# Kernel tuning notes

Hardware: AMD Instinct MI355X
Metric: run time of the kernel (lower is better)

The kernel has to match this reference:

```python
import jax, jax.numpy as jnp
import numpy as np

H, W = 32, 32
S = H * W            # 1024 tokens
B = 16
C = 256              # in_channels == out_channels
HEAD_DIM = 32
N_HEADS = C // HEAD_DIM      # 8
DIM = N_HEADS * HEAD_DIM     # 256
SCALE = DIM ** (-0.5)        # NOTE: full dim, as in the source


def _relative_position_index(h, w):
    # Faithful port of get_relative_position_index (numpy, static)
    coords = np.stack(np.meshgrid(np.arange(h), np.arange(w), indexing='ij'))  # [2,h,w]
    coords_flat = coords.reshape(2, -1)                                        # [2,S]
    rel = coords_flat[:, :, None] - coords_flat[:, None, :]                    # [2,S,S]
    rel = rel.transpose(1, 2, 0).copy()                                        # [S,S,2]
    rel[:, :, 0] += h - 1
    rel[:, :, 1] += w - 1
    rel[:, :, 0] *= 2 * w - 1
    return rel.sum(-1).reshape(-1).astype(np.int32)                            # [S*S]


def setup_inputs() -> dict:
    key = jax.random.key(0)
    ks = jax.random.split(key, 6)
    x = jax.random.normal(ks[0], (B, S, C), dtype=jnp.float32)
    w_qkv = jax.random.normal(ks[1], (3 * DIM, C), dtype=jnp.float32) * 0.02
    b_qkv = jnp.zeros((3 * DIM,), dtype=jnp.float32)
    w_merge = jax.random.normal(ks[2], (C, DIM), dtype=jnp.float32) * 0.02
    b_merge = jnp.zeros((C,), dtype=jnp.float32)
    rel_table = jax.random.normal(ks[3], ((2 * H - 1) * (2 * W - 1), N_HEADS), dtype=jnp.float32) * 0.02
    rel_index = jnp.asarray(_relative_position_index(H, W))  # [S*S] int32
    return {"x": x, "w_qkv": w_qkv, "b_qkv": b_qkv,
            "w_merge": w_merge, "b_merge": b_merge,
            "rel_table": rel_table, "rel_index": rel_index}


def reference(x, w_qkv, b_qkv, w_merge, b_merge, rel_table, rel_index):
    b = x.shape[0]
    qkv = x @ w_qkv.T + b_qkv                       # [B,S,3*DIM]
    q, k, v = jnp.split(qkv, 3, axis=-1)
    def heads(t):
        return t.reshape(b, S, N_HEADS, HEAD_DIM).transpose(0, 2, 1, 3)  # [B,H,S,D]
    q, k, v = heads(q), heads(k), heads(v)
    score = jnp.einsum('bhqd,bhkd->bhqk', q, k) * SCALE   # [B,H,S,S]
    # Faithful to source: torch.gather with index [S*S,1] reads column 0 only
    pos_bias = rel_table[rel_index, 0].reshape(1, 1, S, S)
    attn = jax.nn.softmax(score + pos_bias, axis=-1)
    out = jnp.einsum('bhqk,bhkd->bqhd', attn, v).reshape(b, S, DIM)
    return out @ w_merge.T + b_merge                # [B,S,C]
```

## Files before the change

### kernel.cpp

```cpp
#include <hip/hip_runtime.h>


typedef __attribute__((ext_vector_type(8))) short bf16x8;
typedef __attribute__((ext_vector_type(4))) float f32x4;

#define INV_LN2 1.44269504088896340736f

__device__ __forceinline__ unsigned short f2bf(float f) {
  union { float f; unsigned u; } v; v.f = f;
  unsigned r = v.u + 0x7fffu + ((v.u >> 16) & 1u);
  return (unsigned short)(r >> 16);
}
__device__ __forceinline__ float bf2f(unsigned short h) {
  union { unsigned u; float f; } v; v.u = ((unsigned)h) << 16;
  return v.f;
}

__global__ __launch_bounds__(256) void prep_kernel(
    const float* __restrict__ x, const float* __restrict__ wq,
    const float* __restrict__ wm, const float* __restrict__ tab,
    const int* __restrict__ idx,
    unsigned short* __restrict__ xb, unsigned short* __restrict__ wqb,
    unsigned short* __restrict__ wmb, unsigned short* __restrict__ biasb) {
  const long NX = 1048576, NW1 = 49152, NW2 = 16384, NB = 262144;
  long u = (long)blockIdx.x * 256 + threadIdx.x;
  if (u < NX) {
    float4 v = ((const float4*)x)[u];
    ushort4 o; o.x = f2bf(v.x); o.y = f2bf(v.y); o.z = f2bf(v.z); o.w = f2bf(v.w);
    ((ushort4*)xb)[u] = o;
  } else if (u < NX + NW1) {
    long t = u - NX;
    float4 v = ((const float4*)wq)[t];
    ushort4 o; o.x = f2bf(v.x); o.y = f2bf(v.y); o.z = f2bf(v.z); o.w = f2bf(v.w);
    ((ushort4*)wqb)[t] = o;
  } else if (u < NX + NW1 + NW2) {
    long t = u - NX - NW1;
    float4 v = ((const float4*)wm)[t];
    ushort4 o; o.x = f2bf(v.x); o.y = f2bf(v.y); o.z = f2bf(v.z); o.w = f2bf(v.w);
    ((ushort4*)wmb)[t] = o;
  } else if (u < NX + NW1 + NW2 + NB) {
    long t = (u - NX - NW1 - NW2) * 4;
    int4 iv = ((const int4*)idx)[(u - NX - NW1 - NW2)];
    ushort4 o;
    o.x = f2bf(tab[(long)iv.x * 8] * INV_LN2);
    o.y = f2bf(tab[(long)iv.y * 8] * INV_LN2);
    o.z = f2bf(tab[(long)iv.z * 8] * INV_LN2);
    o.w = f2bf(tab[(long)iv.w * 8] * INV_LN2);
    ((ushort4*)biasb)[t / 4] = o;
  }
}

template <int MODE>
__global__ __launch_bounds__(256) void gemm_k(
    const unsigned short* __restrict__ A, const unsigned short* __restrict__ Bw,
    const float* __restrict__ bias,
    unsigned short* __restrict__ q_ws, unsigned short* __restrict__ k_ws,
    unsigned short* __restrict__ v_ws, float* __restrict__ out) {
  __shared__ unsigned short As[128 * 32];
  __shared__ unsigned short Bs[128 * 32];
  const int tid = threadIdx.x;
  const int lane = tid & 63, wid = tid >> 6;
  const int wm = wid >> 1, wn = wid & 1;
  const int li = lane & 15, g = lane >> 4;
  const int m0 = blockIdx.y * 128;
  const int n0 = blockIdx.x * 128;
  f32x4 acc[4][4] = {};
  const int srow = tid >> 2, sg = tid & 3;
  const unsigned short* Ag = A + (long)(m0 + srow) * 256 + sg * 8;
  const unsigned short* Bg = Bw + (long)(n0 + srow) * 256 + sg * 8;

  for (int kt = 0; kt < 8; ++kt) {
    const int k0 = kt * 32;
    bf16x8 a0 = *(const bf16x8*)(Ag + k0);
    bf16x8 a1 = *(const bf16x8*)(Ag + 64 * 256 + k0);
    bf16x8 b0 = *(const bf16x8*)(Bg + k0);
    bf16x8 b1 = *(const bf16x8*)(Bg + 64 * 256 + k0);
    __syncthreads();
    ((bf16x8*)As)[tid] = a0;
    ((bf16x8*)As)[256 + tid] = a1;
    ((bf16x8*)Bs)[tid] = b0;
    ((bf16x8*)Bs)[256 + tid] = b1;
    __syncthreads();
    bf16x8 af[4], bfr[4];
#pragma unroll
    for (int mi = 0; mi < 4; mi++)
      af[mi] = *(const bf16x8*)(As + (wm * 64 + mi * 16 + li) * 32 + g * 8);
#pragma unroll
    for (int ni = 0; ni < 4; ni++)
      bfr[ni] = *(const bf16x8*)(Bs + (wn * 64 + ni * 16 + li) * 32 + g * 8);
#pragma unroll
    for (int mi = 0; mi < 4; mi++)
#pragma unroll
      for (int ni = 0; ni < 4; ni++)
        acc[mi][ni] = __builtin_amdgcn_mfma_f32_16x16x32_bf16(af[mi], bfr[ni], acc[mi][ni], 0, 0, 0);
  }

  if (MODE == 0) {
    const int sec = n0 >> 8;
    unsigned short* dst = (sec == 0) ? q_ws : ((sec == 1) ? k_ws : v_ws);
#pragma unroll
    for (int mi = 0; mi < 4; mi++)
#pragma unroll
      for (int ni = 0; ni < 4; ni++)
#pragma unroll
        for (int i = 0; i < 4; i++) {
          int m = m0 + wm * 64 + mi * 16 + g * 4 + i;
          int n = n0 + wn * 64 + ni * 16 + li;
          float val = acc[mi][ni][i] + bias[n];
          if (sec == 0) val *= 0.0625f;
          int h = (n >> 5) & 7, d = n & 31;
          int b = m >> 10, s = m & 1023;
          dst[((long)(b * 8 + h) * 1024 + s) * 32 + d] = f2bf(val);
        }
  } else {
#pragma unroll
    for (int mi = 0; mi < 4; mi++)
#pragma unroll
      for (int ni = 0; ni < 4; ni++)
#pragma unroll
        for (int i = 0; i < 4; i++) {
          int m = m0 + wm * 64 + mi * 16 + g * 4 + i;
          int n = n0 + wn * 64 + ni * 16 + li;
          out[(long)m * 256 + n] = acc[mi][ni][i] + bias[n];
        }
  }
}

__global__ __launch_bounds__(256) void attn_kernel(
    const unsigned short* __restrict__ q_ws, const unsigned short* __restrict__ k_ws,
    const unsigned short* __restrict__ v_ws, const unsigned short* __restrict__ biasb,
    unsigned short* __restrict__ attno) {
  __shared__ unsigned short Ks[64 * 32];
  __shared__ unsigned short Vt[32 * 64];
  __shared__ unsigned short Ps[4][16 * 72];
  const int tid = threadIdx.x;
  const int lane = tid & 63, wid = tid >> 6;
  const int li = lane & 15, g = lane >> 4;
  const int bh = blockIdx.y;
  const int q0 = blockIdx.x * 64 + wid * 16;
  const unsigned short* qb = q_ws + (long)bh * 1024 * 32;
  const unsigned short* kb = k_ws + (long)bh * 1024 * 32;
  const unsigned short* vb = v_ws + (long)bh * 1024 * 32;

  bf16x8 qf = *(const bf16x8*)(qb + (q0 + li) * 32 + g * 8);

  f32x4 o0 = {}, o1 = {};
  float lsum[4] = {0.f, 0.f, 0.f, 0.f};
  const int vtok = tid >> 2, vd0 = (tid & 3) * 8;
  const int vswz = (tid & 3) << 4;

  for (int kv0 = 0; kv0 < 1024; kv0 += 64) {
    bf16x8 kv8 = *(const bf16x8*)(kb + (kv0 + (tid >> 2)) * 32 + (tid & 3) * 8);
    bf16x8 vv8 = *(const bf16x8*)(vb + (kv0 + vtok) * 32 + vd0);
    __syncthreads();
    ((bf16x8*)Ks)[tid] = kv8;
#pragma unroll
    for (int j = 0; j < 8; j++) {
      int byteoff = (vd0 + j) * 128 + ((vtok * 2) ^ vswz);
      *(unsigned short*)((char*)Vt + byteoff) = (unsigned short)(unsigned)(unsigned short)vv8[j];
    }
    __syncthreads();

    f32x4 sc[4];
#pragma unroll
    for (int c = 0; c < 4; c++) {
      bf16x8 kf = *(const bf16x8*)(Ks + (c * 16 + li) * 32 + g * 8);
      f32x4 z = {};
      sc[c] = __builtin_amdgcn_mfma_f32_16x16x32_bf16(qf, kf, z, 0, 0, 0);
    }

#pragma unroll
    for (int c = 0; c < 4; c++)
#pragma unroll
      for (int i = 0; i < 4; i++) {
        int qrow = g * 4 + i;
        float bl2 = bf2f(biasb[(long)(q0 + qrow) * 1024 + kv0 + c * 16 + li]);
        float p = exp2f(fmaf(sc[c][i], INV_LN2, bl2));
        lsum[i] += p;
        Ps[wid][qrow * 72 + c * 16 + li] = f2bf(p);
      }

#pragma unroll
    for (int c2 = 0; c2 < 2; c2++) {
      bf16x8 pa = *(const bf16x8*)(&Ps[wid][li * 72 + c2 * 32 + g * 8]);
#pragma unroll
      for (int dblk = 0; dblk < 2; dblk++) {
        int d = li + dblk * 16;
        int byteoff = d * 128 + ((c2 * 64 + g * 16) ^ (((d >> 3) & 3) << 4));
        bf16x8 vf = *(const bf16x8*)((char*)Vt + byteoff);
        if (dblk == 0)
          o0 = __builtin_amdgcn_mfma_f32_16x16x32_bf16(pa, vf, o0, 0, 0, 0);
        else
          o1 = __builtin_amdgcn_mfma_f32_16x16x32_bf16(pa, vf, o1, 0, 0, 0);
      }
    }
  }

#pragma unroll
  for (int i = 0; i < 4; i++) {
    float v = lsum[i];
    v += __shfl_xor(v, 1, 64);
    v += __shfl_xor(v, 2, 64);
    v += __shfl_xor(v, 4, 64);
    v += __shfl_xor(v, 8, 64);
    lsum[i] = v;
  }
  const int b = bh >> 3, h = bh & 7;
#pragma unroll
  for (int i = 0; i < 4; i++) {
    int srow = q0 + g * 4 + i;
    float inv = 1.0f / lsum[i];
    long base = ((long)(b * 1024 + srow)) * 256 + h * 32;
    attno[base + li] = f2bf(o0[i] * inv);
    attno[base + 16 + li] = f2bf(o1[i] * inv);
  }
}

extern "C" void kernel_launch(void* const* d_in, const int* in_sizes, int n_in,
                              void* d_out, int out_size, void* d_ws, size_t ws_size,
                              hipStream_t stream) {
  const float* x      = (const float*)d_in[0];
  const float* wqkv   = (const float*)d_in[1];
  const float* bqkv   = (const float*)d_in[2];
  const float* wmerge = (const float*)d_in[3];
  const float* bmerge = (const float*)d_in[4];
  const float* rtab   = (const float*)d_in[5];
  const int*   ridx   = (const int*)d_in[6];
  float* out = (float*)d_out;

  char* ws = (char*)d_ws;
  unsigned short* xb    = (unsigned short*)(ws);
  unsigned short* wqb   = (unsigned short*)(ws + 8388608);
  unsigned short* wmb   = (unsigned short*)(ws + 8781824);
  unsigned short* biasb = (unsigned short*)(ws + 8912896);
  unsigned short* q_ws  = (unsigned short*)(ws + 11010048);
  unsigned short* k_ws  = (unsigned short*)(ws + 19398656);
  unsigned short* v_ws  = (unsigned short*)(ws + 27787264);
  unsigned short* attno = (unsigned short*)(ws + 36175872);

  prep_kernel<<<5376, 256, 0, stream>>>(x, wqkv, wmerge, rtab, ridx, xb, wqb, wmb, biasb);
  gemm_k<0><<<dim3(6, 128), 256, 0, stream>>>(xb, wqb, bqkv, q_ws, k_ws, v_ws, nullptr);
  attn_kernel<<<dim3(16, 128), 256, 0, stream>>>(q_ws, k_ws, v_ws, biasb, attno);
  gemm_k<1><<<dim3(2, 128), 256, 0, stream>>>(attno, wmb, bmerge, nullptr, nullptr, nullptr, out);
}
```

Baseline: 109.6 us.

## Pre-transpose V, stage bias in LDS, fold softmax sums into MFMA

Adds a separate kernel that writes V transposed into the workspace, so attention loads V tiles with vector reads instead of scattered 16-bit LDS stores. The positional bias is loaded into LDS with coalesced vector loads and fed as the initial MFMA accumulator, and the 1/ln2 factor is folded into the Q scaling so exp2 can be applied directly. Row sums are computed by an extra MFMA against a ones vector, and P is packed with v_cvt_pk_bf16_f32. GEMM and attention LDS tiles are padded to reduce bank conflicts. The cost is one extra kernel launch plus a full pass over V in global memory.

```diff
diff --git a/kernel.cpp b/kernel.cpp
--- a/kernel.cpp
+++ b/kernel.cpp
@@ -39,14 +39,14 @@
     ushort4 o; o.x = f2bf(v.x); o.y = f2bf(v.y); o.z = f2bf(v.z); o.w = f2bf(v.w);
     ((ushort4*)wmb)[t] = o;
   } else if (u < NX + NW1 + NW2 + NB) {
-    long t = (u - NX - NW1 - NW2) * 4;
-    int4 iv = ((const int4*)idx)[(u - NX - NW1 - NW2)];
+    long t = u - NX - NW1 - NW2;
+    int4 iv = ((const int4*)idx)[t];
     ushort4 o;
     o.x = f2bf(tab[(long)iv.x * 8] * INV_LN2);
     o.y = f2bf(tab[(long)iv.y * 8] * INV_LN2);
     o.z = f2bf(tab[(long)iv.z * 8] * INV_LN2);
     o.w = f2bf(tab[(long)iv.w * 8] * INV_LN2);
-    ((ushort4*)biasb)[t / 4] = o;
+    ((ushort4*)biasb)[t] = o;
   }
 }
 
@@ -56,8 +56,8 @@
     const float* __restrict__ bias,
     unsigned short* __restrict__ q_ws, unsigned short* __restrict__ k_ws,
     unsigned short* __restrict__ v_ws, float* __restrict__ out) {
-  __shared__ unsigned short As[128 * 32];
-  __shared__ unsigned short Bs[128 * 32];
+  __shared__ __align__(16) unsigned short As[128 * 40];
+  __shared__ __align__(16) unsigned short Bs[128 * 40];
   const int tid = threadIdx.x;
   const int lane = tid & 63, wid = tid >> 6;
   const int wm = wid >> 1, wn = wid & 1;
@@ -76,18 +76,18 @@
     bf16x8 b0 = *(const bf16x8*)(Bg + k0);
     bf16x8 b1 = *(const bf16x8*)(Bg + 64 * 256 + k0);
     __syncthreads();
-    ((bf16x8*)As)[tid] = a0;
-    ((bf16x8*)As)[256 + tid] = a1;
-    ((bf16x8*)Bs)[tid] = b0;
-    ((bf16x8*)Bs)[256 + tid] = b1;
+    *(bf16x8*)(As + srow * 40 + sg * 8) = a0;
+    *(bf16x8*)(As + (srow + 64) * 40 + sg * 8) = a1;
+    *(bf16x8*)(Bs + srow * 40 + sg * 8) = b0;
+    *(bf16x8*)(Bs + (srow + 64) * 40 + sg * 8) = b1;
     __syncthreads();
     bf16x8 af[4], bfr[4];
 #pragma unroll
     for (int mi = 0; mi < 4; mi++)
-      af[mi] = *(const bf16x8*)(As + (wm * 64 + mi * 16 + li) * 32 + g * 8);
+      af[mi] = *(const bf16x8*)(As + (wm * 64 + mi * 16 + li) * 40 + g * 8);
 #pragma unroll
     for (int ni = 0; ni < 4; ni++)
-      bfr[ni] = *(const bf16x8*)(Bs + (wn * 64 + ni * 16 + li) * 32 + g * 8);
+      bfr[ni] = *(const bf16x8*)(Bs + (wn * 64 + ni * 16 + li) * 40 + g * 8);
 #pragma unroll
     for (int mi = 0; mi < 4; mi++)
 #pragma unroll
@@ -98,6 +98,7 @@
   if (MODE == 0) {
     const int sec = n0 >> 8;
     unsigned short* dst = (sec == 0) ? q_ws : ((sec == 1) ? k_ws : v_ws);
+    const float qscale = 0.0625f * INV_LN2;
 #pragma unroll
     for (int mi = 0; mi < 4; mi++)
 #pragma unroll
@@ -107,7 +108,7 @@
           int m = m0 + wm * 64 + mi * 16 + g * 4 + i;
           int n = n0 + wn * 64 + ni * 16 + li;
           float val = acc[mi][ni][i] + bias[n];
-          if (sec == 0) val *= 0.0625f;
+          if (sec == 0) val *= qscale;
           int h = (n >> 5) & 7, d = n & 31;
           int b = m >> 10, s = m & 1023;
           dst[((long)(b * 8 + h) * 1024 + s) * 32 + d] = f2bf(val);
@@ -126,90 +127,109 @@
   }
 }
 
+__global__ __launch_bounds__(256) void vtrans_kernel(
+    const unsigned short* __restrict__ v, unsigned short* __restrict__ vt) {
+  long u = (long)blockIdx.x * 256 + threadIdx.x;
+  if (u >= 524288) return;
+  int tok_lin = (int)(u >> 2);
+  int dchunk = ((int)u & 3) * 8;
+  int bh = tok_lin >> 10, s = tok_lin & 1023;
+  bf16x8 r = *(const bf16x8*)(v + (long)tok_lin * 32 + dchunk);
+  unsigned short* base = vt + (long)bh * 32768 + s;
+#pragma unroll
+  for (int j = 0; j < 8; j++) base[(long)(dchunk + j) * 1024] = (unsigned short)r[j];
+}
+
 __global__ __launch_bounds__(256) void attn_kernel(
     const unsigned short* __restrict__ q_ws, const unsigned short* __restrict__ k_ws,
-    const unsigned short* __restrict__ v_ws, const unsigned short* __restrict__ biasb,
+    const unsigned short* __restrict__ vt_ws, const unsigned short* __restrict__ biasb,
     unsigned short* __restrict__ attno) {
-  __shared__ unsigned short Ks[64 * 32];
-  __shared__ unsigned short Vt[32 * 64];
-  __shared__ unsigned short Ps[4][16 * 72];
+  __shared__ __align__(16) unsigned short Ks[64 * 40];
+  __shared__ __align__(16) unsigned short Vt[32 * 72];
+  __shared__ __align__(16) unsigned short Bi[64 * 72];
+  __shared__ __align__(16) unsigned short Ps[4][16 * 72];
   const int tid = threadIdx.x;
   const int lane = tid & 63, wid = tid >> 6;
   const int li = lane & 15, g = lane >> 4;
   const int bh = blockIdx.y;
-  const int q0 = blockIdx.x * 64 + wid * 16;
-  const unsigned short* qb = q_ws + (long)bh * 1024 * 32;
-  const unsigned short* kb = k_ws + (long)bh * 1024 * 32;
-  const unsigned short* vb = v_ws + (long)bh * 1024 * 32;
+  const int qblk = blockIdx.x * 64;
+  const int q0 = qblk + wid * 16;
+  const unsigned short* qb = q_ws + (long)bh * 32768;
+  const unsigned short* kb = k_ws + (long)bh * 32768;
+  const unsigned short* vb = vt_ws + (long)bh * 32768;
 
   bf16x8 qf = *(const bf16x8*)(qb + (q0 + li) * 32 + g * 8);
 
-  f32x4 o0 = {}, o1 = {};
-  float lsum[4] = {0.f, 0.f, 0.f, 0.f};
-  const int vtok = tid >> 2, vd0 = (tid & 3) * 8;
-  const int vswz = (tid & 3) << 4;
+  bf16x8 onesf = {};
+  if (li == 0) {
+#pragma unroll
+    for (int j = 0; j < 8; j++) onesf[j] = (short)0x3F80;
+  }
+
+  f32x4 o0 = {}, o1 = {}, o2 = {};
+  const int kt = tid >> 2, kd = (tid & 3) * 8;
+  const int vd = tid >> 3, vs = (tid & 7) * 8;
+  const int bq = tid >> 2, bt = (tid & 3) * 16;
+  unsigned short* Pw = Ps[wid];
 
   for (int kv0 = 0; kv0 < 1024; kv0 += 64) {
-    bf16x8 kv8 = *(const bf16x8*)(kb + (kv0 + (tid >> 2)) * 32 + (tid & 3) * 8);
-    bf16x8 vv8 = *(const bf16x8*)(vb + (kv0 + vtok) * 32 + vd0);
-    __syncthreads();
-    ((bf16x8*)Ks)[tid] = kv8;
-#pragma unroll
-    for (int j = 0; j < 8; j++) {
-      int byteoff = (vd0 + j) * 128 + ((vtok * 2) ^ vswz);
-      *(unsigned short*)((char*)Vt + byteoff) = (unsigned short)(unsigned)(unsigned short)vv8[j];
+    bf16x8 kv8 = *(const bf16x8*)(kb + (kv0 + kt) * 32 + kd);
+    bf16x8 vv8 = *(const bf16x8*)(vb + vd * 1024 + kv0 + vs);
+    bf16x8 bb0 = *(const bf16x8*)(biasb + (long)(qblk + bq) * 1024 + kv0 + bt);
+    bf16x8 bb1 = *(const bf16x8*)(biasb + (long)(qblk + bq) * 1024 + kv0 + bt + 8);
+    __syncthreads();
+    *(bf16x8*)(Ks + kt * 40 + kd) = kv8;
+    *(bf16x8*)(Vt + vd * 72 + vs) = vv8;
+    *(bf16x8*)(Bi + bq * 72 + bt) = bb0;
+    *(bf16x8*)(Bi + bq * 72 + bt + 8) = bb1;
+    __syncthreads();
+
+    f32x4 sc[4];
+#pragma unroll
+    for (int c = 0; c < 4; c++) {
+      const unsigned short* brow = Bi + (wid * 16 + g * 4) * 72 + c * 16 + li;
+      f32x4 ci;
+      ci[0] = bf2f(brow[0]);
+      ci[1] = bf2f(brow[72]);
+      ci[2] = bf2f(brow[144]);
+      ci[3] = bf2f(brow[216]);
+      bf16x8 kf = *(const bf16x8*)(Ks + (c * 16 + li) * 40 + g * 8);
+      sc[c] = __builtin_amdgcn_mfma_f32_16x16x32_bf16(qf, kf, ci, 0, 0, 0);
     }
-    __syncthreads();
-
-    f32x4 sc[4];
+
 #pragma unroll
     for (int c = 0; c < 4; c++) {
-      bf16x8 kf = *(const bf16x8*)(Ks + (c * 16 + li) * 32 + g * 8);
-      f32x4 z = {};
-      sc[c] = __builtin_amdgcn_mfma_f32_16x16x32_bf16(qf, kf, z, 0, 0, 0);
+      float p0 = exp2f(sc[c][0]);
+      float p1 = exp2f(sc[c][1]);
+      float p2 = exp2f(sc[c][2]);
+      float p3 = exp2f(sc[c][3]);
+      unsigned r01, r23;
+      asm("v_cvt_pk_bf16_f32 %0, %1, %2" : "=v"(r01) : "v"(p0), "v"(p1));
+      asm("v_cvt_pk_bf16_f32 %0, %1, %2" : "=v"(r23) : "v"(p2), "v"(p3));
+      unsigned short* pb = Pw + (g * 4) * 72 + c * 16 + li;
+      pb[0]   = (unsigned short)(r01 & 0xffffu);
+      pb[72]  = (unsigned short)(r01 >> 16);
+      pb[144] = (unsigned short)(r23 & 0xffffu);
+      pb[216] = (unsigned short)(r23 >> 16);
     }
 
 #pragma unroll
-    for (int c = 0; c < 4; c++)
-#pragma unroll
-      for (int i = 0; i < 4; i++) {
-        int qrow = g * 4 + i;
-        float bl2 = bf2f(biasb[(long)(q0 + qrow) * 1024 + kv0 + c * 16 + li]);
-        float p = exp2f(fmaf(sc[c][i], INV_LN2, bl2));
-        lsum[i] += p;
-        Ps[wid][qrow * 72 + c * 16 + li] = f2bf(p);
-      }
-
-#pragma unroll
     for (int c2 = 0; c2 < 2; c2++) {
-      bf16x8 pa = *(const bf16x8*)(&Ps[wid][li * 72 + c2 * 32 + g * 8]);
-#pragma unroll
-      for (int dblk = 0; dblk < 2; dblk++) {
-        int d = li + dblk * 16;
-        int byteoff = d * 128 + ((c2 * 64 + g * 16) ^ (((d >> 3) & 3) << 4));
-        bf16x8 vf = *(const bf16x8*)((char*)Vt + byteoff);
-        if (dblk == 0)
-          o0 = __builtin_amdgcn_mfma_f32_16x16x32_bf16(pa, vf, o0, 0, 0, 0);
-        else
-          o1 = __builtin_amdgcn_mfma_f32_16x16x32_bf16(pa, vf, o1, 0, 0, 0);
-      }
+      bf16x8 pa  = *(const bf16x8*)(Pw + li * 72 + c2 * 32 + g * 8);
+      bf16x8 vf0 = *(const bf16x8*)(Vt + li * 72 + c2 * 32 + g * 8);
+      bf16x8 vf1 = *(const bf16x8*)(Vt + (li + 16) * 72 + c2 * 32 + g * 8);
+      o0 = __builtin_amdgcn_mfma_f32_16x16x32_bf16(pa, vf0, o0, 0, 0, 0);
+      o1 = __builtin_amdgcn_mfma_f32_16x16x32_bf16(pa, vf1, o1, 0, 0, 0);
+      o2 = __builtin_amdgcn_mfma_f32_16x16x32_bf16(pa, onesf, o2, 0, 0, 0);
     }
   }
 
+  const int b = bh >> 3, h = bh & 7;
 #pragma unroll
   for (int i = 0; i < 4; i++) {
-    float v = lsum[i];
-    v += __shfl_xor(v, 1, 64);
-    v += __shfl_xor(v, 2, 64);
-    v += __shfl_xor(v, 4, 64);
-    v += __shfl_xor(v, 8, 64);
-    lsum[i] = v;
-  }
-  const int b = bh >> 3, h = bh & 7;
-#pragma unroll
-  for (int i = 0; i < 4; i++) {
+    float s = __shfl(o2[i], lane & 48, 64);
+    float inv = 1.0f / s;
     int srow = q0 + g * 4 + i;
-    float inv = 1.0f / lsum[i];
     long base = ((long)(b * 1024 + srow)) * 256 + h * 32;
     attno[base + li] = f2bf(o0[i] * inv);
     attno[base + 16 + li] = f2bf(o1[i] * inv);
@@ -237,9 +257,11 @@
   unsigned short* k_ws  = (unsigned short*)(ws + 19398656);
   unsigned short* v_ws  = (unsigned short*)(ws + 27787264);
   unsigned short* attno = (unsigned short*)(ws + 36175872);
+  unsigned short* vt_ws = xb;
 
   prep_kernel<<<5376, 256, 0, stream>>>(x, wqkv, wmerge, rtab, ridx, xb, wqb, wmb, biasb);
   gemm_k<0><<<dim3(6, 128), 256, 0, stream>>>(xb, wqb, bqkv, q_ws, k_ws, v_ws, nullptr);
-  attn_kernel<<<dim3(16, 128), 256, 0, stream>>>(q_ws, k_ws, v_ws, biasb, attno);
+  vtrans_kernel<<<2048, 256, 0, stream>>>(v_ws, vt_ws);
+  attn_kernel<<<dim3(16, 128), 256, 0, stream>>>(q_ws, k_ws, vt_ws, biasb, attno);
   gemm_k<1><<<dim3(2, 128), 256, 0, stream>>>(attno, wmb, bmerge, nullptr, nullptr, nullptr, out);
 }
```

Measured after the change: 117.4 us. +7.1%, slower.
